# Kernel optimization log

Hardware: AMD Instinct MI355X
Metric: run time of the kernel (lower is better)

Reference implementation:

```python
import jax, jax.numpy as jnp
import numpy as np

B, S = 64, 512
CHAR_V, WORD_V = 8000, 100000
CE = WE = 256
D = 256            # gated conv channel dim (config.char_embed_size)
PE = CE + WE       # pos_embed_size must equal concat dim
P = 50             # predicate_num
DILS = (1, 2, 5, 1, 2, 5, 1, 2, 5, 1, 1, 1)
BN_EPS = 1e-3      # keras BatchNormalization default epsilon


def setup_inputs() -> dict:
    key = jax.random.key(0)
    k = jax.random.split(key, 12)
    s = 0.02
    return {
        "inputs": jax.random.randint(k[0], (B, S), 0, CHAR_V),
        "inputs_word": jax.random.randint(k[1], (B, S), 0, WORD_V),
        "inputs_position": jnp.broadcast_to(jnp.arange(S), (B, S)),
        "input_sub_loc": jnp.sort(jax.random.randint(k[2], (B, 2), 0, S), axis=1),
        "char_table": jax.random.normal(k[3], (CHAR_V, CE)) * s,
        "word_table": jax.random.normal(k[4], (WORD_V, WE)) * s,
        "pos_table": jax.random.normal(k[5], (S, PE)) * s,
        "conv_w1": jax.random.normal(k[6], (3, PE, 2 * D)) / np.sqrt(3.0 * PE),
        "conv_b1": jnp.zeros((2 * D,), jnp.float32),
        "conv_w": jax.random.normal(k[7], (11, 3, D, 2 * D)) / np.sqrt(3.0 * D),
        "conv_b": jnp.zeros((11, 2 * D), jnp.float32),
        "sub_w": jax.random.normal(k[8], (D, 2)) / np.sqrt(float(D)),
        "sub_b": jnp.zeros((2,), jnp.float32),
        "po_w": jax.random.normal(k[9], (3 * D, 2 * P)) / np.sqrt(3.0 * D),
        "po_b": jnp.zeros((2 * P,), jnp.float32),
        "bn_gamma": jnp.ones((3 * D,), jnp.float32),
        "bn_beta": jnp.zeros((3 * D,), jnp.float32),
    }


def _dgc(x, mask, w, b, dil):
    # dilated gated conv1d: conv -> split into gate/value -> gated residual -> mask
    h = jax.lax.conv_general_dilated(
        x, w, window_strides=(1,), padding="SAME", rhs_dilation=(dil,),
        dimension_numbers=("NWC", "WIO", "NWC")) + b
    g = jax.nn.sigmoid(h[..., :D])
    hv = h[..., D:]
    if x.shape[-1] != D:          # first layer projects PE -> D, no residual
        out = hv * g
    else:
        out = x * (1.0 - g) + hv * g
    return out * mask


def reference(inputs, inputs_word, inputs_position, input_sub_loc,
              char_table, word_table, pos_table,
              conv_w1, conv_b1, conv_w, conv_b,
              sub_w, sub_b, po_w, po_b, bn_gamma, bn_beta):
    # embeddings: concat(char, word) + pos   -> [B, S, PE]
    embed = jnp.concatenate([char_table[inputs], word_table[inputs_word]],
                            axis=-1) + pos_table[inputs_position]
    mask_bool = inputs != 0
    mask = mask_bool[..., None].astype(embed.dtype)  # [B, S, 1]

    x = _dgc(embed, mask, conv_w1, conv_b1, DILS[0])
    for i in range(11):
        x = _dgc(x, mask, conv_w[i], conv_b[i], DILS[i + 1])  # [B, S, D]

    sub_preds = jax.nn.sigmoid(jnp.einsum("bsd,dk->bsk", x, sub_w) + sub_b)

    # seq_gather of subject start/end vectors
    bidx = jnp.arange(B)
    sub_start = x[bidx, input_sub_loc[:, 0]]  # [B, D]
    sub_end = x[bidx, input_sub_loc[:, 1]]    # [B, D]
    vec = jnp.concatenate([sub_start, sub_end], axis=-1)  # [B, 2D]

    # seq_and_vec: broadcast vec over seq dim and concat -> [B, S, 3D]
    feat = jnp.concatenate(
        [x, jnp.broadcast_to(vec[:, None, :], (B, S, 2 * D))], axis=-1)

    # BatchNorm (training mode: batch statistics over (batch, seq))
    mu = jnp.mean(feat, axis=(0, 1))
    var = jnp.var(feat, axis=(0, 1))
    feat = (feat - mu) * jax.lax.rsqrt(var + BN_EPS) * bn_gamma + bn_beta

    po_preds = jax.nn.sigmoid(jnp.einsum("bsf,fp->bsp", feat, po_w) + po_b)

    return (jnp.transpose(sub_preds, (0, 2, 1)),   # [B, 2, S]
            jnp.transpose(po_preds, (0, 2, 1)),    # [B, 2P, S]
            mask_bool)
```

## Files before the change

### kernel.cpp

```cpp
#include <hip/hip_runtime.h>
#include <hip/hip_bf16.h>

typedef __attribute__((ext_vector_type(8))) short bf16x8;
typedef __attribute__((ext_vector_type(4))) float f32x4;

#define B_   64
#define S_   512
#define M_   32768
#define D_   256

__device__ __forceinline__ float b2f(unsigned short u) {
    union { unsigned int i; float f; } v; v.i = ((unsigned int)u) << 16; return v.f;
}
__device__ __forceinline__ unsigned short f2b(float f) {
    union { float f; unsigned int i; } v; v.f = f;
    unsigned int x = v.i;
    return (unsigned short)((x + 0x7fffu + ((x >> 16) & 1u)) >> 16);
}
__device__ __forceinline__ float sigm(float x) { return 1.f / (1.f + __expf(-x)); }

__device__ __forceinline__ float ldany(const void* p, size_t i, int f32) {
    return f32 ? ((const float*)p)[i] : b2f(((const unsigned short*)p)[i]);
}

__device__ __forceinline__ int omap(int o) {
    int half = o >> 8, d = o & 255;
    return ((d >> 4) * 32) + half * 16 + (d & 15);
}
__device__ __forceinline__ int omap_inv(int n) {
    int grp = n >> 5, half = (n >> 4) & 1, dlow = n & 15;
    return half * 256 + grp * 16 + dlow;
}

__global__ void k_detect(const void* sample, int* flag) {
    __shared__ int s;
    int t = threadIdx.x;
    if (t == 0) s = 0;
    __syncthreads();
    const unsigned short* u = (const unsigned short*)sample;
    float a = fabsf(b2f(u[2 * t]));
    if (!(a < 1e3f)) atomicOr(&s, 1);
    __syncthreads();
    if (t == 0) *flag = s;
}

__global__ __launch_bounds__(256)
void k_embed(const int* __restrict__ ids_c, const int* __restrict__ ids_w,
             const int* __restrict__ ids_p,
             const void* __restrict__ char_t,
             const void* __restrict__ word_t,
             const void* __restrict__ pos_t,
             unsigned short* __restrict__ embed,
             float* __restrict__ maskf,
             void* __restrict__ outv,
             const int* __restrict__ flag) {
    const int f32 = *flag;
    const int t = threadIdx.x;
    const int pos = blockIdx.x * 4 + (t >> 6);
    const int ch0 = (t & 63) * 8;
    const int c = ids_c[pos], w = ids_w[pos], p = ids_p[pos];
    if ((t & 63) == 0) {
        float m = (c != 0) ? 1.f : 0.f;
        maskf[pos] = m;
        size_t eidx = 65536 + 3276800 + (size_t)pos;
        if (f32) ((float*)outv)[eidx] = m;
        else ((unsigned short*)outv)[eidx] = f2b(m);
    }
    float tab[8], pe[8];
    const int in_char = (ch0 < 256);
    const size_t tidx = in_char ? ((size_t)c * 256 + ch0) : ((size_t)w * 256 + (ch0 - 256));
    const void* tp = in_char ? char_t : word_t;
    if (f32) {
        const float4 a0 = *(const float4*)((const float*)tp + tidx);
        const float4 a1 = *(const float4*)((const float*)tp + tidx + 4);
        tab[0]=a0.x; tab[1]=a0.y; tab[2]=a0.z; tab[3]=a0.w;
        tab[4]=a1.x; tab[5]=a1.y; tab[6]=a1.z; tab[7]=a1.w;
        const float4 b0 = *(const float4*)((const float*)pos_t + (size_t)p * 512 + ch0);
        const float4 b1 = *(const float4*)((const float*)pos_t + (size_t)p * 512 + ch0 + 4);
        pe[0]=b0.x; pe[1]=b0.y; pe[2]=b0.z; pe[3]=b0.w;
        pe[4]=b1.x; pe[5]=b1.y; pe[6]=b1.z; pe[7]=b1.w;
    } else {
        const unsigned short* tu = (const unsigned short*)tp + tidx;
        const unsigned short* pu = (const unsigned short*)pos_t + (size_t)p * 512 + ch0;
        uint4 av = *(const uint4*)tu;
        uint4 bv = *(const uint4*)pu;
        const unsigned short* as = (const unsigned short*)&av;
        const unsigned short* bs = (const unsigned short*)&bv;
#pragma unroll
        for (int i = 0; i < 8; ++i) { tab[i] = b2f(as[i]); pe[i] = b2f(bs[i]); }
    }
    unsigned short o[8];
#pragma unroll
    for (int i = 0; i < 8; ++i) o[i] = f2b(tab[i] + pe[i]);
    *(uint4*)(embed + (size_t)pos * 512 + ch0) = *(uint4*)o;
}

__global__ void k_repack(const void* __restrict__ w1,
                         const void* __restrict__ w11,
                         const void* __restrict__ b1,
                         const void* __restrict__ b11,
                         unsigned short* __restrict__ w1p,
                         unsigned short* __restrict__ wp,
                         float* __restrict__ biasP,
                         const int* __restrict__ flag) {
    const int f32 = *flag;
    const int T1 = 3 * 512 * 512 / 8;
    const int T2 = 11 * 3 * 512 * 256 / 8;
    const int T3 = 12 * 512;
    const int total = T1 + T2 + T3;
    for (int idx = blockIdx.x * blockDim.x + threadIdx.x; idx < total;
         idx += gridDim.x * blockDim.x) {
        if (idx < T1) {
            int row = idx >> 6;
            int c0 = (idx & 63) * 8;
            int tap = row >> 9, n = row & 511;
            int o = omap_inv(n);
            unsigned short v[8];
#pragma unroll
            for (int i = 0; i < 8; ++i)
                v[i] = f2b(ldany(w1, (size_t)tap * 262144 + (size_t)(c0 + i) * 512 + o, f32));
            *(uint4*)(w1p + ((size_t)row << 9) + c0) = *(uint4*)v;
        } else if (idx < T1 + T2) {
            int j = idx - T1;
            int row = j >> 5;
            int c0 = (j & 31) * 8;
            int lt = row >> 9, n = row & 511;
            int o = omap_inv(n);
            unsigned short v[8];
#pragma unroll
            for (int i = 0; i < 8; ++i)
                v[i] = f2b(ldany(w11, (size_t)lt * 131072 + (size_t)(c0 + i) * 512 + o, f32));
            *(uint4*)(wp + ((size_t)row << 8) + c0) = *(uint4*)v;
        } else {
            int j = idx - T1 - T2;
            if (j < 512) {
                biasP[omap(j)] = ldany(b1, j, f32);
            } else {
                int jj = j - 512;
                int lay = jj >> 9, o = jj & 511;
                biasP[512 + lay * 512 + omap(o)] = ldany(b11, jj, f32);
            }
        }
    }
}

template <int CIN, bool RES>
__global__ __launch_bounds__(256)
void k_dgc(const unsigned short* __restrict__ xin,
           const unsigned short* __restrict__ wT,
           const float* __restrict__ bias,
           const float* __restrict__ maskf,
           unsigned short* __restrict__ xout,
           int dil) {
    __shared__ unsigned short ldsA[138 * 64];
    __shared__ unsigned short ldsB[128 * 64];
    const int id = blockIdx.x;
    const int xcd = id & 7, sl = id >> 3;
    const int mt = xcd * 32 + (sl >> 2);
    const int nt = sl & 3;
    const int m0 = mt * 128, n0 = nt * 128;
    const int b = m0 >> 9, s0 = m0 & 511;
    const int t = threadIdx.x;
    const int lane = t & 63, wv = t >> 6;
    const int wm = wv >> 1, wn = wv & 1;
    const int lm = lane & 15, lq = lane >> 4;
    const int NR = 128 + 2 * dil;

    f32x4 acc[4][4];
#pragma unroll
    for (int i = 0; i < 4; i++)
#pragma unroll
        for (int j = 0; j < 4; j++)
#pragma unroll
            for (int e = 0; e < 4; e++) acc[i][j][e] = 0.f;

    for (int k0 = 0; k0 < CIN; k0 += 64) {
        __syncthreads();
        for (int i = t; i < NR * 8; i += 256) {
            int row = i >> 3, q = i & 7;
            int sp = s0 - dil + row;
            uint4 va = make_uint4(0u, 0u, 0u, 0u);
            if (sp >= 0 && sp < S_)
                va = *(const uint4*)(xin + (size_t)(b * S_ + sp) * CIN + k0 + q * 8);
            *(uint4*)(ldsA + row * 64 + ((q ^ (row & 7)) * 8)) = va;
        }
        for (int tap = 0; tap < 3; ++tap) {
            if (tap > 0) __syncthreads();
            const unsigned short* wtap = wT + ((size_t)tap * 512 + n0) * CIN;
#pragma unroll
            for (int i0 = 0; i0 < 4; ++i0) {
                int i = t + i0 * 256;
                int row = i >> 3, q = i & 7;
                uint4 vb = *(const uint4*)(wtap + (size_t)row * CIN + k0 + q * 8);
                *(uint4*)(ldsB + row * 64 + ((q ^ (row & 7)) * 8)) = vb;
            }
            __syncthreads();
            const int rbase = wm * 64 + tap * dil;
#pragma unroll
            for (int kk = 0; kk < 2; ++kk) {
                bf16x8 af[4], bfr[4];
#pragma unroll
                for (int mi = 0; mi < 4; ++mi) {
                    int er = rbase + mi * 16 + lm;
                    af[mi] = *(const bf16x8*)(ldsA + er * 64 + (((kk * 4 + lq) ^ (er & 7)) * 8));
                }
#pragma unroll
                for (int ni = 0; ni < 4; ++ni) {
                    int br = wn * 64 + ni * 16 + lm;
                    bfr[ni] = *(const bf16x8*)(ldsB + br * 64 + (((kk * 4 + lq) ^ (br & 7)) * 8));
                }
#pragma unroll
                for (int mi = 0; mi < 4; ++mi)
#pragma unroll
                    for (int ni = 0; ni < 4; ++ni)
                        acc[mi][ni] = __builtin_amdgcn_mfma_f32_16x16x32_bf16(
                            af[mi], bfr[ni], acc[mi][ni], 0, 0, 0);
            }
        }
    }

    const int colbase = n0 + wn * 64;
#pragma unroll
    for (int mi = 0; mi < 4; ++mi) {
#pragma unroll
        for (int p = 0; p < 2; ++p) {
            const int d = (colbase >> 1) + p * 16 + lm;
            const int ng = colbase + p * 32 + lm;
            const float bg = bias[ng], bv = bias[ng + 16];
#pragma unroll
            for (int r = 0; r < 4; ++r) {
                const int m = m0 + wm * 64 + mi * 16 + lq * 4 + r;
                float hg = acc[mi][2 * p][r] + bg;
                float hv = acc[mi][2 * p + 1][r] + bv;
                float g = sigm(hg);
                float o = hv * g;
                if (RES) {
                    float xi = b2f(xin[(size_t)m * CIN + d]);
                    o = xi * (1.f - g) + hv * g;
                }
                o *= maskf[m];
                xout[(size_t)m * 256 + d] = f2b(o);
            }
        }
    }
}

__global__ void k_vec(const unsigned short* __restrict__ x, const int* __restrict__ loc,
                      float* __restrict__ vec) {
    int b = blockIdx.x;
    int j = threadIdx.x;
    int which = j >> 8, d = j & 255;
    int s = loc[b * 2 + which];
    vec[b * 512 + j] = b2f(x[((size_t)(b * 512 + s)) * 256 + d]);
}

__global__ void k_zero(float* __restrict__ stats) { stats[threadIdx.x] = 0.f; }

__global__ void k_stats(const unsigned short* __restrict__ x, float* __restrict__ stats) {
    int c = threadIdx.x;
    int base = blockIdx.x * 128;
    float s = 0.f, q = 0.f;
    for (int r = 0; r < 128; ++r) {
        float v = b2f(x[(size_t)(base + r) * 256 + c]);
        s += v; q += v * v;
    }
    atomicAdd(&stats[c], s);
    atomicAdd(&stats[256 + c], q);
}

__global__ void k_final(const float* __restrict__ stats, const float* __restrict__ vec,
                        const void* __restrict__ gamma,
                        const void* __restrict__ beta,
                        float* __restrict__ scale, float* __restrict__ shift,
                        const int* __restrict__ flag) {
    const int f32 = *flag;
    int f = threadIdx.x;
    float mu, var;
    if (f < 256) {
        mu = stats[f] * (1.f / 32768.f);
        var = stats[256 + f] * (1.f / 32768.f) - mu * mu;
    } else {
        float s = 0.f, q = 0.f;
        int j = f - 256;
        for (int b = 0; b < 64; ++b) {
            float v = vec[b * 512 + j];
            s += v; q += v * v;
        }
        mu = s * (1.f / 64.f);
        var = q * (1.f / 64.f) - mu * mu;
    }
    float sc = ldany(gamma, f, f32) * rsqrtf(var + 1e-3f);
    scale[f] = sc;
    shift[f] = ldany(beta, f, f32) - mu * sc;
}

__global__ void k_prep1(const float* __restrict__ scale, const void* __restrict__ po_w,
                        const void* __restrict__ sub_w,
                        unsigned short* __restrict__ pwT,
                        const int* __restrict__ flag) {
    const int f32 = *flag;
    int idx = blockIdx.x * blockDim.x + threadIdx.x;
    int n = idx >> 8, k = idx & 255;
    float v = 0.f;
    if (n < 100) v = scale[k] * ldany(po_w, (size_t)k * 100 + n, f32);
    else if (n < 102) v = ldany(sub_w, (size_t)k * 2 + (n - 100), f32);
    pwT[n * 256 + k] = f2b(v);
}

__global__ __launch_bounds__(256)
void k_cmat(const float* __restrict__ scale, const float* __restrict__ shift,
            const float* __restrict__ vec,
            const void* __restrict__ po_w,
            const void* __restrict__ po_b,
            const void* __restrict__ sub_b,
            float* __restrict__ Cmat,
            const int* __restrict__ flag) {
    const int f32 = *flag;
    const int wid = blockIdx.x * 4 + (threadIdx.x >> 6);
    const int lane = threadIdx.x & 63;
    const int b = wid / 102, n = wid - b * 102;
    if (b >= 64) return;
    if (n >= 100) {
        if (lane == 0) Cmat[b * 128 + n] = ldany(sub_b, n - 100, f32);
        return;
    }
    float partial = 0.f;
#pragma unroll
    for (int f = lane; f < 768; f += 64) {
        float term = shift[f];
        if (f >= 256) term += vec[b * 512 + (f - 256)] * scale[f];
        partial += term * ldany(po_w, (size_t)f * 100 + n, f32);
    }
#pragma unroll
    for (int off = 32; off > 0; off >>= 1)
        partial += __shfl_xor(partial, off);
    if (lane == 0) Cmat[b * 128 + n] = partial + ldany(po_b, n, f32);
}

__global__ __launch_bounds__(256)
void k_po(const unsigned short* __restrict__ x,
          const unsigned short* __restrict__ pwT,
          const float* __restrict__ Cmat,
          void* __restrict__ outv,
          const int* __restrict__ flag) {
    const int f32 = *flag;
    __shared__ unsigned short ldsA[128 * 40];
    __shared__ unsigned short ldsB[128 * 40];
    const int mt = blockIdx.x;
    const int m0 = mt * 128;
    const int b = m0 >> 9;
    const int t = threadIdx.x;
    const int lane = t & 63, wv = t >> 6;
    const int wm = wv >> 1, wn = wv & 1;
    const int lm = lane & 15, lq = lane >> 4;

    f32x4 acc[4][4];
#pragma unroll
    for (int i = 0; i < 4; i++)
#pragma unroll
        for (int j = 0; j < 4; j++)
#pragma unroll
            for (int e = 0; e < 4; e++) acc[i][j][e] = 0.f;

    for (int k0 = 0; k0 < 256; k0 += 32) {
        __syncthreads();
#pragma unroll
        for (int a0 = 0; a0 < 2; ++a0) {
            int a = t + a0 * 256;
            int row = a >> 2, q = a & 3;
            uint4 va = *(const uint4*)(x + (size_t)(m0 + row) * 256 + k0 + q * 8);
            *(uint4*)(ldsA + row * 40 + q * 8) = va;
            uint4 vb = *(const uint4*)(pwT + (size_t)row * 256 + k0 + q * 8);
            *(uint4*)(ldsB + row * 40 + q * 8) = vb;
        }
        __syncthreads();
        bf16x8 af[4], bfr[4];
#pragma unroll
        for (int mi = 0; mi < 4; ++mi)
            af[mi] = *(const bf16x8*)(ldsA + (wm * 64 + mi * 16 + lm) * 40 + lq * 8);
#pragma unroll
        for (int ni = 0; ni < 4; ++ni)
            bfr[ni] = *(const bf16x8*)(ldsB + (wn * 64 + ni * 16 + lm) * 40 + lq * 8);
#pragma unroll
        for (int mi = 0; mi < 4; ++mi)
#pragma unroll
            for (int ni = 0; ni < 4; ++ni)
                acc[mi][ni] = __builtin_amdgcn_mfma_f32_16x16x32_bf16(
                    af[mi], bfr[ni], acc[mi][ni], 0, 0, 0);
    }

#pragma unroll
    for (int mi = 0; mi < 4; ++mi)
#pragma unroll
        for (int ni = 0; ni < 4; ++ni) {
            const int n = wn * 64 + ni * 16 + lm;
            const float cc = Cmat[b * 128 + n];
#pragma unroll
            for (int r = 0; r < 4; ++r) {
                const int m = m0 + wm * 64 + mi * 16 + lq * 4 + r;
                const int s = m & 511;
                float v = sigm(acc[mi][ni][r] + cc);
                if (n < 102) {
                    size_t eidx;
                    if (n < 100) eidx = 65536 + (((size_t)b * 100 + n) * 512 + s);
                    else eidx = ((size_t)b * 2 + (n - 100)) * 512 + s;
                    if (f32) ((float*)outv)[eidx] = v;
                    else ((unsigned short*)outv)[eidx] = f2b(v);
                }
            }
        }
}

extern "C" void kernel_launch(void* const* d_in, const int* in_sizes, int n_in,
                              void* d_out, int out_size, void* d_ws, size_t ws_size,
                              hipStream_t stream) {
    const int* ids_c = (const int*)d_in[0];
    const int* ids_w = (const int*)d_in[1];
    const int* ids_p = (const int*)d_in[2];
    const int* loc = (const int*)d_in[3];
    const void* char_t = d_in[4];
    const void* word_t = d_in[5];
    const void* pos_t = d_in[6];
    const void* w1 = d_in[7];
    const void* b1 = d_in[8];
    const void* w11 = d_in[9];
    const void* b11 = d_in[10];
    const void* sub_w = d_in[11];
    const void* sub_b = d_in[12];
    const void* po_w = d_in[13];
    const void* po_b = d_in[14];
    const void* gamma = d_in[15];
    const void* beta = d_in[16];

    char* ws = (char*)d_ws;
    unsigned short* embed = (unsigned short*)(ws + 0);
    unsigned short* xA = (unsigned short*)(ws + 33554432);
    unsigned short* xB = (unsigned short*)(ws + 50331648);
    unsigned short* w1p = (unsigned short*)(ws + 67108864);
    unsigned short* wp = (unsigned short*)(ws + 68681728);
    float* biasP = (float*)(ws + 77332480);
    float* maskf = (float*)(ws + 77357056);
    float* vec = (float*)(ws + 77488128);
    float* stats = (float*)(ws + 77619200);
    float* scale = (float*)(ws + 77621248);
    float* shift = (float*)(ws + 77624320);
    unsigned short* pwT = (unsigned short*)(ws + 77627392);
    float* Cmat = (float*)(ws + 77692928);
    int* dflag = (int*)(ws + 77725696);

    k_detect<<<1, 256, 0, stream>>>(word_t, dflag);
    k_zero<<<1, 512, 0, stream>>>(stats);
    k_embed<<<8192, 256, 0, stream>>>(ids_c, ids_w, ids_p, char_t, word_t, pos_t,
                                      embed, maskf, d_out, dflag);
    k_repack<<<2560, 256, 0, stream>>>(w1, w11, b1, b11, w1p, wp, biasP, dflag);

    k_dgc<512, false><<<1024, 256, 0, stream>>>(embed, w1p, biasP, maskf, xA, 1);

    const int dils[12] = {1, 2, 5, 1, 2, 5, 1, 2, 5, 1, 1, 1};
    unsigned short* xi = xA;
    unsigned short* xo = xB;
    for (int i = 1; i < 12; ++i) {
        k_dgc<256, true><<<1024, 256, 0, stream>>>(
            xi, wp + (size_t)(i - 1) * 3 * 512 * 256, biasP + i * 512, maskf, xo, dils[i]);
        unsigned short* tmp = xi; xi = xo; xo = tmp;
    }

    k_vec<<<64, 512, 0, stream>>>(xi, loc, vec);
    k_stats<<<256, 256, 0, stream>>>(xi, stats);
    k_final<<<1, 768, 0, stream>>>(stats, vec, gamma, beta, scale, shift, dflag);
    k_prep1<<<128, 256, 0, stream>>>(scale, po_w, sub_w, pwT, dflag);
    k_cmat<<<1632, 256, 0, stream>>>(scale, shift, vec, po_w, po_b, sub_b, Cmat, dflag);
    k_po<<<256, 256, 0, stream>>>(xi, pwT, Cmat, d_out, dflag);
}
```

Baseline: 775.8 us.

## Load activations directly from global, stage all three weight taps with register prefetch

The activation tile is no longer staged through LDS. Each wave now loads its A fragments straight from global memory, with bounds checks for the dilated taps. All three weight taps for a K-chunk are staged into one larger LDS buffer at once, and the next chunk is prefetched into registers so the per-tap barriers go away. Occupancy is hinted at 3 blocks per CU. The trade is more register pressure and uncoalesced, repeated global reads of activations (each row is read for 3 taps and by both N-waves) against fewer syncs and better overlap.

```diff
diff --git a/kernel.cpp b/kernel.cpp
--- a/kernel.cpp
+++ b/kernel.cpp
@@ -145,15 +145,14 @@
 }
 
 template <int CIN, bool RES>
-__global__ __launch_bounds__(256)
+__global__ __launch_bounds__(256, 3)
 void k_dgc(const unsigned short* __restrict__ xin,
            const unsigned short* __restrict__ wT,
            const float* __restrict__ bias,
            const float* __restrict__ maskf,
            unsigned short* __restrict__ xout,
            int dil) {
-    __shared__ unsigned short ldsA[138 * 64];
-    __shared__ unsigned short ldsB[128 * 64];
+    __shared__ unsigned short ldsB[3 * 128 * 64];
     const int id = blockIdx.x;
     const int xcd = id & 7, sl = id >> 3;
     const int mt = xcd * 32 + (sl >> 2);
@@ -164,7 +163,17 @@
     const int lane = t & 63, wv = t >> 6;
     const int wm = wv >> 1, wn = wv & 1;
     const int lm = lane & 15, lq = lane >> 4;
-    const int NR = 128 + 2 * dil;
+
+    int bls[12];
+    const unsigned short* bgp[12];
+#pragma unroll
+    for (int i0 = 0; i0 < 12; ++i0) {
+        int i = t + i0 * 256;
+        int tap = i >> 10, rem = i & 1023;
+        int row = rem >> 3, q = rem & 7;
+        bls[i0] = (tap * 128 + row) * 64 + ((q ^ (row & 7)) * 8);
+        bgp[i0] = wT + ((size_t)tap * 512 + n0 + row) * CIN + q * 8;
+    }
 
     f32x4 acc[4][4];
 #pragma unroll
@@ -173,41 +182,43 @@
         for (int j = 0; j < 4; j++)
 #pragma unroll
             for (int e = 0; e < 4; e++) acc[i][j][e] = 0.f;
+
+    uint4 pB[12];
+#pragma unroll
+    for (int i0 = 0; i0 < 12; ++i0) pB[i0] = *(const uint4*)(bgp[i0]);
+
+    const unsigned short* xrow = xin + (size_t)b * S_ * CIN;
 
     for (int k0 = 0; k0 < CIN; k0 += 64) {
         __syncthreads();
-        for (int i = t; i < NR * 8; i += 256) {
-            int row = i >> 3, q = i & 7;
-            int sp = s0 - dil + row;
-            uint4 va = make_uint4(0u, 0u, 0u, 0u);
-            if (sp >= 0 && sp < S_)
-                va = *(const uint4*)(xin + (size_t)(b * S_ + sp) * CIN + k0 + q * 8);
-            *(uint4*)(ldsA + row * 64 + ((q ^ (row & 7)) * 8)) = va;
-        }
+#pragma unroll
+        for (int i0 = 0; i0 < 12; ++i0)
+            *(uint4*)(ldsB + bls[i0]) = pB[i0];
+        __syncthreads();
+        if (k0 + 64 < CIN) {
+#pragma unroll
+            for (int i0 = 0; i0 < 12; ++i0)
+                pB[i0] = *(const uint4*)(bgp[i0] + k0 + 64);
+        }
+#pragma unroll
         for (int tap = 0; tap < 3; ++tap) {
-            if (tap > 0) __syncthreads();
-            const unsigned short* wtap = wT + ((size_t)tap * 512 + n0) * CIN;
-#pragma unroll
-            for (int i0 = 0; i0 < 4; ++i0) {
-                int i = t + i0 * 256;
-                int row = i >> 3, q = i & 7;
-                uint4 vb = *(const uint4*)(wtap + (size_t)row * CIN + k0 + q * 8);
-                *(uint4*)(ldsB + row * 64 + ((q ^ (row & 7)) * 8)) = vb;
-            }
-            __syncthreads();
-            const int rbase = wm * 64 + tap * dil;
+            const int roff = (tap - 1) * dil;
 #pragma unroll
             for (int kk = 0; kk < 2; ++kk) {
                 bf16x8 af[4], bfr[4];
 #pragma unroll
                 for (int mi = 0; mi < 4; ++mi) {
-                    int er = rbase + mi * 16 + lm;
-                    af[mi] = *(const bf16x8*)(ldsA + er * 64 + (((kk * 4 + lq) ^ (er & 7)) * 8));
+                    const int sp = s0 + wm * 64 + mi * 16 + lm + roff;
+                    bf16x8 z = {0, 0, 0, 0, 0, 0, 0, 0};
+                    if (sp >= 0 && sp < S_)
+                        z = *(const bf16x8*)(xrow + (size_t)sp * CIN + k0 + kk * 32 + lq * 8);
+                    af[mi] = z;
                 }
 #pragma unroll
                 for (int ni = 0; ni < 4; ++ni) {
-                    int br = wn * 64 + ni * 16 + lm;
-                    bfr[ni] = *(const bf16x8*)(ldsB + br * 64 + (((kk * 4 + lq) ^ (br & 7)) * 8));
+                    const int br = wn * 64 + ni * 16 + lm;
+                    bfr[ni] = *(const bf16x8*)(ldsB + (tap * 128 + br) * 64 +
+                                               (((kk * 4 + lq) ^ (br & 7)) * 8));
                 }
 #pragma unroll
                 for (int mi = 0; mi < 4; ++mi)
```

Measured after the change: 1.996 ms. +157.3%, slower.
